# Performance work log

Measured on AMD Instinct MI355X. Metric: run time of the kernel, lower is better.

Reference implementation:

```python
import jax, jax.numpy as jnp
import numpy as np

N = 100000   # nodes (batched graph)
E = 1600000  # edges
G = 2048     # molecules in the batch
D_IN = 128
D_H = 128
MLP_H = 512


def setup_inputs() -> dict:
    key = jax.random.key(0)
    ks = jax.random.split(key, 20)

    def w(k, i, o):
        return (jax.random.normal(k, (i, o), jnp.float32) / np.sqrt(i)).astype(jnp.float32)

    feats = jax.random.normal(ks[0], (N, D_IN), jnp.float32)
    src = jax.random.randint(ks[1], (E,), 0, N)
    dst = jax.random.randint(ks[2], (E,), 0, N)
    graph_ids = jnp.sort(jax.random.randint(ks[3], (N,), 0, G))

    return {
        "feats": feats, "src": src, "dst": dst, "graph_ids": graph_ids,
        # 3 GraphConv layers
        "W0": w(ks[4], D_IN, D_H), "b0": jnp.zeros((D_H,), jnp.float32),
        "W1": w(ks[5], D_H, D_H),  "b1": jnp.zeros((D_H,), jnp.float32),
        "W2": w(ks[6], D_H, D_H),  "b2": jnp.zeros((D_H,), jnp.float32),
        # MLP head: D_H -> 512 -> 256 -> 1
        "Wm0": w(ks[7], D_H, MLP_H),       "bm0": jnp.zeros((MLP_H,), jnp.float32),
        "Wm1": w(ks[8], MLP_H, MLP_H // 2), "bm1": jnp.zeros((MLP_H // 2,), jnp.float32),
        "Wm2": w(ks[9], MLP_H // 2, 1),     "bm2": jnp.zeros((1,), jnp.float32),
    }


def reference(feats, src, dst, graph_ids, W0, b0, W1, b1, W2, b2,
              Wm0, bm0, Wm1, bm1, Wm2, bm2):
    ones_e = jnp.ones((E,), jnp.float32)
    # DGL GraphConv norm='both': D_out^{-1/2} on src, D_in^{-1/2} on dst; deg clamped to 1
    deg_out = jnp.maximum(jax.ops.segment_sum(ones_e, src, num_segments=N), 1.0)
    deg_in = jnp.maximum(jax.ops.segment_sum(ones_e, dst, num_segments=N), 1.0)
    inv_src = jax.lax.rsqrt(deg_out)[:, None]
    inv_dst = jax.lax.rsqrt(deg_in)[:, None]

    def gcn_layer(h, W, b):
        h = h * inv_src                                   # [N, D]
        m = jax.ops.segment_sum(h[src], dst, num_segments=N)  # gather-scatter over edges
        m = m * inv_dst
        return jax.nn.relu(jnp.dot(m, W) + b)

    h = gcn_layer(feats, W0, b0)
    h = gcn_layer(h, W1, b1)
    h = gcn_layer(h, W2, b2)

    # AvgPooling per graph
    counts = jnp.maximum(jax.ops.segment_sum(jnp.ones((N,), jnp.float32), graph_ids, num_segments=G), 1.0)
    emb = jax.ops.segment_sum(h, graph_ids, num_segments=G) / counts[:, None]  # [G, D_H]

    # MLP head (dropout = identity in eval)
    x = jax.nn.relu(jnp.dot(emb, Wm0) + bm0)
    x = jax.nn.relu(jnp.dot(x, Wm1) + bm1)
    return jnp.dot(x, Wm2) + bm2  # [G, 1]
```

## Files before the change

kernel.cpp:

```cpp
#include <hip/hip_runtime.h>


static inline int ceil_div(int a, int b){ return (a + b - 1) / b; }

#define B1 128
#define NBMAX 1024

__global__ __launch_bounds__(256) void bucket_count_kernel(
    const int* __restrict__ src, const int* __restrict__ dst,
    unsigned* __restrict__ cntA, unsigned* __restrict__ cntB,
    int E, int NB){
  __shared__ unsigned la[NBMAX], lb[NBMAX];
  int t = threadIdx.x;
  for (int i = t; i < NB; i += 256){ la[i] = 0u; lb[i] = 0u; }
  __syncthreads();
  int chunk = (E + B1 - 1) / B1;
  int e0 = blockIdx.x * chunk, e1 = min(e0 + chunk, E);
  for (int e = e0 + t; e < e1; e += 256){
    atomicAdd(&la[dst[e] >> 7], 1u);
    atomicAdd(&lb[src[e] >> 7], 1u);
  }
  __syncthreads();
  for (int i = t; i < NB; i += 256){
    cntA[(size_t)blockIdx.x * NB + i] = la[i];
    cntB[(size_t)blockIdx.x * NB + i] = lb[i];
  }
}

__global__ void scan_cols_kernel(unsigned* __restrict__ cntA, unsigned* __restrict__ cntB,
                                 unsigned* __restrict__ totals, int NB){
  int b = blockIdx.x * 256 + threadIdx.x;
  if (b >= NB) return;
  unsigned* cnt = blockIdx.y ? cntB : cntA;
  unsigned run = 0;
  for (int blk = 0; blk < B1; blk++){
    unsigned v = cnt[(size_t)blk * NB + b];
    cnt[(size_t)blk * NB + b] = run;
    run += v;
  }
  totals[(size_t)blockIdx.y * NB + b] = run;
}

__global__ void scan_base_kernel(const unsigned* __restrict__ totals,
                                 unsigned* __restrict__ baseA, unsigned* __restrict__ baseB,
                                 int NB, int E){
  __shared__ unsigned s[NBMAX];
  int t = threadIdx.x;
  for (int job = 0; job < 2; job++){
    unsigned* base = job ? baseB : baseA;
    unsigned x = (t < NB) ? totals[(size_t)job * NB + t] : 0u;
    s[t] = x;
    __syncthreads();
    for (int off = 1; off < NBMAX; off <<= 1){
      unsigned v = (t >= off) ? s[t - off] : 0u;
      __syncthreads();
      s[t] += v;
      __syncthreads();
    }
    if (t < NB) base[t] = s[t] - x;
    if (t == 0) base[NB] = (unsigned)E;
    __syncthreads();
  }
}

__global__ __launch_bounds__(256) void bucket_scatter_kernel(
    const int* __restrict__ src, const int* __restrict__ dst,
    const unsigned* __restrict__ cntA, const unsigned* __restrict__ cntB,
    const unsigned* __restrict__ baseA, const unsigned* __restrict__ baseB,
    int* __restrict__ bsrc_d, int* __restrict__ bdst_d, int* __restrict__ bsrc_s,
    int E, int NB){
  __shared__ unsigned curA[NBMAX], curB[NBMAX];
  int t = threadIdx.x;
  for (int i = t; i < NB; i += 256){
    curA[i] = baseA[i] + cntA[(size_t)blockIdx.x * NB + i];
    curB[i] = baseB[i] + cntB[(size_t)blockIdx.x * NB + i];
  }
  __syncthreads();
  int chunk = (E + B1 - 1) / B1;
  int e0 = blockIdx.x * chunk, e1 = min(e0 + chunk, E);
  for (int e = e0 + t; e < e1; e += 256){
    int s = src[e], d = dst[e];
    unsigned p = atomicAdd(&curA[d >> 7], 1u);
    bsrc_d[p] = s;
    bdst_d[p] = d;
    unsigned q = atomicAdd(&curB[s >> 7], 1u);
    bsrc_s[q] = s;
  }
}

__global__ __launch_bounds__(256) void csr_finalize_kernel(
    const int* __restrict__ bsrc_d, const int* __restrict__ bdst_d,
    const unsigned* __restrict__ baseA,
    int* __restrict__ row_ptr, float* __restrict__ inv_dst, int* __restrict__ col,
    int N, int E, int NB){
  __shared__ unsigned cnt[128];
  __shared__ unsigned scn[128];
  int b = blockIdx.x, t = threadIdx.x;
  int node0 = b << 7;
  int nn = min(128, N - node0);
  int e0 = (int)baseA[b], e1 = (int)baseA[b + 1];
  if (t < 128) cnt[t] = 0u;
  __syncthreads();
  for (int e = e0 + t; e < e1; e += 256)
    atomicAdd(&cnt[bdst_d[e] & 127], 1u);
  __syncthreads();
  unsigned mycnt = (t < 128) ? cnt[t] : 0u;
  if (t < 128) scn[t] = mycnt;
  __syncthreads();
  for (int off = 1; off < 128; off <<= 1){
    unsigned v = (t < 128 && t >= off) ? scn[t - off] : 0u;
    __syncthreads();
    if (t < 128) scn[t] += v;
    __syncthreads();
  }
  if (t < nn){
    unsigned excl = scn[t] - mycnt;
    row_ptr[node0 + t] = e0 + (int)excl;
    unsigned c = mycnt < 1u ? 1u : mycnt;
    inv_dst[node0 + t] = rsqrtf((float)c);
    cnt[t] = (unsigned)e0 + excl;
  }
  if (b == NB - 1 && t == 0) row_ptr[N] = E;
  __syncthreads();
  for (int e = e0 + t; e < e1; e += 256){
    unsigned p = atomicAdd(&cnt[bdst_d[e] & 127], 1u);
    col[p] = bsrc_d[e];
  }
}

__global__ __launch_bounds__(256) void degout_finalize_kernel(
    const int* __restrict__ bsrc_s, const unsigned* __restrict__ baseB,
    float* __restrict__ inv_src, int N){
  __shared__ unsigned cnt[128];
  int b = blockIdx.x, t = threadIdx.x;
  int node0 = b << 7;
  int nn = min(128, N - node0);
  int e0 = (int)baseB[b], e1 = (int)baseB[b + 1];
  if (t < 128) cnt[t] = 0u;
  __syncthreads();
  for (int e = e0 + t; e < e1; e += 256)
    atomicAdd(&cnt[bsrc_s[e] & 127], 1u);
  __syncthreads();
  if (t < nn){
    unsigned c = cnt[t] < 1u ? 1u : cnt[t];
    inv_src[node0 + t] = rsqrtf((float)c);
  }
}

__global__ void scale_rows_kernel(const float* __restrict__ in, const float* __restrict__ sc,
                                  float* __restrict__ out, int n4){
  int i = blockIdx.x*blockDim.x + threadIdx.x;
  if (i < n4){
    float4 v = ((const float4*)in)[i];
    float s = sc[i >> 5];
    v.x *= s; v.y *= s; v.z *= s; v.w *= s;
    ((float4*)out)[i] = v;
  }
}

__global__ __launch_bounds__(256) void csr_agg_kernel(
    const int* __restrict__ row_ptr, const int* __restrict__ col,
    const float* __restrict__ hs, float* __restrict__ agg, int N){
  int w = (int)((blockIdx.x*256u + threadIdx.x) >> 6);
  int lane = threadIdx.x & 63;
  if (w >= N) return;
  int r0 = __builtin_amdgcn_readfirstlane(row_ptr[w]);
  int r1 = __builtin_amdgcn_readfirstlane(row_ptr[w+1]);
  float ax0=0.f, ay0=0.f, ax1=0.f, ay1=0.f;
  float ax2=0.f, ay2=0.f, ax3=0.f, ay3=0.f;
  int e = r0;
  for (; e + 3 < r1; e += 4){
    int s0 = __builtin_amdgcn_readfirstlane(col[e]);
    int s1 = __builtin_amdgcn_readfirstlane(col[e+1]);
    int s2 = __builtin_amdgcn_readfirstlane(col[e+2]);
    int s3 = __builtin_amdgcn_readfirstlane(col[e+3]);
    float2 v0 = ((const float2*)(hs + (size_t)s0*128))[lane];
    float2 v1 = ((const float2*)(hs + (size_t)s1*128))[lane];
    float2 v2 = ((const float2*)(hs + (size_t)s2*128))[lane];
    float2 v3 = ((const float2*)(hs + (size_t)s3*128))[lane];
    ax0 += v0.x; ay0 += v0.y;
    ax1 += v1.x; ay1 += v1.y;
    ax2 += v2.x; ay2 += v2.y;
    ax3 += v3.x; ay3 += v3.y;
  }
  for (; e < r1; e++){
    int s0 = __builtin_amdgcn_readfirstlane(col[e]);
    float2 v0 = ((const float2*)(hs + (size_t)s0*128))[lane];
    ax0 += v0.x; ay0 += v0.y;
  }
  float2 r;
  r.x = (ax0 + ax1) + (ax2 + ax3);
  r.y = (ay0 + ay1) + (ay2 + ay3);
  ((float2*)(agg + (size_t)w*128))[lane] = r;
}

__global__ __launch_bounds__(256) void gemm_kernel(
    const float* __restrict__ A, const float* __restrict__ W,
    const float* __restrict__ bias, const float* __restrict__ row_scale,
    const float* __restrict__ out_scale, float* __restrict__ out,
    int M, int K, int Ncols, int do_relu){
  __shared__ float As[32][68];
  __shared__ float Bs[32][128];

  const int tid = threadIdx.x;
  const int tx = tid & 31;
  const int ty = tid >> 5;
  const int row0 = blockIdx.x * 64;
  const int col0 = blockIdx.y * 128;

  float acc[8][4];
  #pragma unroll
  for (int i = 0; i < 8; i++)
    #pragma unroll
    for (int j = 0; j < 4; j++) acc[i][j] = 0.f;

  for (int kb = 0; kb < K; kb += 32){
    #pragma unroll
    for (int i = 0; i < 2; i++){
      int flat = i*256 + tid;
      int m = flat >> 3, k4 = (flat & 7) << 2;
      int gm = row0 + m;
      float4 v = make_float4(0.f, 0.f, 0.f, 0.f);
      if (gm < M){
        v = *(const float4*)(A + (size_t)gm*K + kb + k4);
        if (row_scale){ float s = row_scale[gm]; v.x*=s; v.y*=s; v.z*=s; v.w*=s; }
      }
      As[k4+0][m] = v.x; As[k4+1][m] = v.y; As[k4+2][m] = v.z; As[k4+3][m] = v.w;
    }
    #pragma unroll
    for (int i = 0; i < 4; i++){
      int flat = i*256 + tid;
      int k = flat >> 5, j4 = (flat & 31) << 2;
      float4 v = *(const float4*)(W + (size_t)(kb + k)*Ncols + col0 + j4);
      *(float4*)&Bs[k][j4] = v;
    }
    __syncthreads();
    #pragma unroll
    for (int k = 0; k < 32; k++){
      float4 b = *(const float4*)&Bs[k][tx << 2];
      float a[8];
      #pragma unroll
      for (int i = 0; i < 8; i++) a[i] = As[k][ty*8 + i];
      #pragma unroll
      for (int i = 0; i < 8; i++){
        acc[i][0] = fmaf(a[i], b.x, acc[i][0]);
        acc[i][1] = fmaf(a[i], b.y, acc[i][1]);
        acc[i][2] = fmaf(a[i], b.z, acc[i][2]);
        acc[i][3] = fmaf(a[i], b.w, acc[i][3]);
      }
    }
    __syncthreads();
  }

  float4 bi = *(const float4*)(bias + col0 + (tx << 2));
  #pragma unroll
  for (int i = 0; i < 8; i++){
    int gm = row0 + ty*8 + i;
    if (gm < M){
      float4 v;
      v.x = acc[i][0] + bi.x; v.y = acc[i][1] + bi.y;
      v.z = acc[i][2] + bi.z; v.w = acc[i][3] + bi.w;
      if (do_relu){
        v.x = fmaxf(v.x, 0.f); v.y = fmaxf(v.y, 0.f);
        v.z = fmaxf(v.z, 0.f); v.w = fmaxf(v.w, 0.f);
      }
      if (out_scale){ float s = out_scale[gm]; v.x*=s; v.y*=s; v.z*=s; v.w*=s; }
      *(float4*)(out + (size_t)gm*Ncols + col0 + (tx << 2)) = v;
    }
  }
}

__global__ void pool_kernel(const float* __restrict__ h, const int* __restrict__ gid,
                            float* __restrict__ emb, int N, int G){
  int g = blockIdx.x;
  int lane = threadIdx.x;
  int lo = 0, hi = N;
  while (lo < hi){ int mid = (lo + hi) >> 1; if (gid[mid] < g) lo = mid + 1; else hi = mid; }
  int start = lo;
  hi = N;
  while (lo < hi){ int mid = (lo + hi) >> 1; if (gid[mid] <= g) lo = mid + 1; else hi = mid; }
  int end = lo;
  float ax = 0.f, ay = 0.f;
  for (int n = start; n < end; n++){
    float2 v = ((const float2*)(h + (size_t)n*128))[lane];
    ax += v.x; ay += v.y;
  }
  int c = end - start; if (c < 1) c = 1;
  float invc = 1.0f / (float)c;
  float2 r; r.x = ax * invc; r.y = ay * invc;
  ((float2*)(emb + (size_t)g*128))[lane] = r;
}

__global__ void final_dot_kernel(const float* __restrict__ x, const float* __restrict__ w,
                                 const float* __restrict__ b, float* __restrict__ out, int G){
  int idx = blockIdx.x*blockDim.x + threadIdx.x;
  int g = idx >> 6, lane = idx & 63;
  if (g >= G) return;
  float4 xv = ((const float4*)(x + (size_t)g*256))[lane];
  float4 wv = ((const float4*)w)[lane];
  float s = xv.x*wv.x + xv.y*wv.y + xv.z*wv.z + xv.w*wv.w;
  for (int off = 32; off > 0; off >>= 1) s += __shfl_down(s, off);
  if (lane == 0) out[g] = s + b[0];
}

extern "C" void kernel_launch(void* const* d_in, const int* in_sizes, int n_in,
                              void* d_out, int out_size, void* d_ws, size_t ws_size,
                              hipStream_t stream){
  const float* feats = (const float*)d_in[0];
  const int*   src   = (const int*)d_in[1];
  const int*   dst   = (const int*)d_in[2];
  const int*   gid   = (const int*)d_in[3];
  const float* W0 = (const float*)d_in[4];   const float* b0 = (const float*)d_in[5];
  const float* W1 = (const float*)d_in[6];   const float* b1 = (const float*)d_in[7];
  const float* W2 = (const float*)d_in[8];   const float* b2 = (const float*)d_in[9];
  const float* Wm0 = (const float*)d_in[10]; const float* bm0 = (const float*)d_in[11];
  const float* Wm1 = (const float*)d_in[12]; const float* bm1 = (const float*)d_in[13];
  const float* Wm2 = (const float*)d_in[14]; const float* bm2 = (const float*)d_in[15];
  float* out = (float*)d_out;

  const int E   = in_sizes[1];
  const int N   = in_sizes[3];
  const int G   = out_size;
  const int MH  = in_sizes[11];
  const int MH2 = in_sizes[13];
  const int NB  = ceil_div(N, 128);

  char* ws = (char*)d_ws;
  size_t off = 0;
  auto carve = [&](size_t bytes) -> char* {
    off = (off + 255) & ~(size_t)255;
    char* p = ws + off; off += bytes; return p;
  };
  float* inv_src = (float*)carve((size_t)N*4);
  float* inv_dst = (float*)carve((size_t)N*4);
  int* row_ptr = (int*)carve((size_t)(N+1)*4);
  int* col     = (int*)carve((size_t)E*4);
  float* hs  = (float*)carve((size_t)N*128*4);
  float* agg = (float*)carve((size_t)N*128*4);
  float* emb = (float*)carve((size_t)G*128*4);
  float* x1  = (float*)carve((size_t)G*MH*4);
  float* x2  = (float*)carve((size_t)G*MH2*4);

  unsigned* T = (unsigned*)agg;
  unsigned* cntA   = T;
  unsigned* cntB   = cntA + (size_t)B1*NB;
  unsigned* totals = cntB + (size_t)B1*NB;
  unsigned* baseA  = totals + 2*(size_t)NB;
  unsigned* baseB  = baseA + (NB+1);
  int* bsrc_d = (int*)(baseB + (NB+1));
  int* bdst_d = bsrc_d + E;
  int* bsrc_s = bdst_d + E;

  bucket_count_kernel<<<B1, 256, 0, stream>>>(src, dst, cntA, cntB, E, NB);
  scan_cols_kernel<<<dim3(ceil_div(NB,256), 2), 256, 0, stream>>>(cntA, cntB, totals, NB);
  scan_base_kernel<<<1, NBMAX, 0, stream>>>(totals, baseA, baseB, NB, E);
  bucket_scatter_kernel<<<B1, 256, 0, stream>>>(src, dst, cntA, cntB, baseA, baseB,
                                                bsrc_d, bdst_d, bsrc_s, E, NB);
  csr_finalize_kernel<<<NB, 256, 0, stream>>>(bsrc_d, bdst_d, baseA, row_ptr, inv_dst, col, N, E, NB);
  degout_finalize_kernel<<<NB, 256, 0, stream>>>(bsrc_s, baseB, inv_src, N);
  scale_rows_kernel<<<ceil_div(N*32,256), 256, 0, stream>>>(feats, inv_src, hs, N*32);

  const int agg_blocks = ceil_div(N*64, 256);
  dim3 ggrid(ceil_div(N,64), 1);
  csr_agg_kernel<<<agg_blocks, 256, 0, stream>>>(row_ptr, col, hs, agg, N);
  gemm_kernel<<<ggrid, 256, 0, stream>>>(agg, W0, b0, inv_dst, inv_src, hs, N, 128, 128, 1);
  csr_agg_kernel<<<agg_blocks, 256, 0, stream>>>(row_ptr, col, hs, agg, N);
  gemm_kernel<<<ggrid, 256, 0, stream>>>(agg, W1, b1, inv_dst, inv_src, hs, N, 128, 128, 1);
  csr_agg_kernel<<<agg_blocks, 256, 0, stream>>>(row_ptr, col, hs, agg, N);
  gemm_kernel<<<ggrid, 256, 0, stream>>>(agg, W2, b2, inv_dst, nullptr, hs, N, 128, 128, 1);
  pool_kernel<<<G, 64, 0, stream>>>(hs, gid, emb, N, G);
  gemm_kernel<<<dim3(ceil_div(G,64), MH/128),  256, 0, stream>>>(emb, Wm0, bm0, nullptr, nullptr, x1, G, 128, MH, 1);
  gemm_kernel<<<dim3(ceil_div(G,64), MH2/128), 256, 0, stream>>>(x1, Wm1, bm1, nullptr, nullptr, x2, G, MH, MH2, 1);
  final_dot_kernel<<<ceil_div(G*64,256), 256, 0, stream>>>(x2, Wm2, bm2, out, G);
}
```

Measured before the change: 825.8 us.

## Fuse CSR neighbor aggregation with dense layer GEMM into one kernel

Replaces the separate CSR aggregation and GEMM kernels per GCN layer with one kernel. Each block first aggregates 64 nodes' neighbor rows into shared memory (transposed, with inv_dst applied), then multiplies by the weight matrix with bias, ReLU and output scaling. The agg buffer is no longer written to and read back from global memory, and three launches are dropped. In exchange the kernel uses a larger shared-memory footprint (about 50KB), which may lower occupancy for the latency-bound gather phase. The GEMM phase now waits on the slowest of the block's 64 gather rows.

```diff
diff --git a/kernel.cpp b/kernel.cpp
--- a/kernel.cpp
+++ b/kernel.cpp
@@ -158,40 +158,103 @@
   }
 }
 
-__global__ __launch_bounds__(256) void csr_agg_kernel(
+__global__ __launch_bounds__(256) void agg_gemm_kernel(
     const int* __restrict__ row_ptr, const int* __restrict__ col,
-    const float* __restrict__ hs, float* __restrict__ agg, int N){
-  int w = (int)((blockIdx.x*256u + threadIdx.x) >> 6);
-  int lane = threadIdx.x & 63;
-  if (w >= N) return;
-  int r0 = __builtin_amdgcn_readfirstlane(row_ptr[w]);
-  int r1 = __builtin_amdgcn_readfirstlane(row_ptr[w+1]);
-  float ax0=0.f, ay0=0.f, ax1=0.f, ay1=0.f;
-  float ax2=0.f, ay2=0.f, ax3=0.f, ay3=0.f;
-  int e = r0;
-  for (; e + 3 < r1; e += 4){
-    int s0 = __builtin_amdgcn_readfirstlane(col[e]);
-    int s1 = __builtin_amdgcn_readfirstlane(col[e+1]);
-    int s2 = __builtin_amdgcn_readfirstlane(col[e+2]);
-    int s3 = __builtin_amdgcn_readfirstlane(col[e+3]);
-    float2 v0 = ((const float2*)(hs + (size_t)s0*128))[lane];
-    float2 v1 = ((const float2*)(hs + (size_t)s1*128))[lane];
-    float2 v2 = ((const float2*)(hs + (size_t)s2*128))[lane];
-    float2 v3 = ((const float2*)(hs + (size_t)s3*128))[lane];
-    ax0 += v0.x; ay0 += v0.y;
-    ax1 += v1.x; ay1 += v1.y;
-    ax2 += v2.x; ay2 += v2.y;
-    ax3 += v3.x; ay3 += v3.y;
-  }
-  for (; e < r1; e++){
-    int s0 = __builtin_amdgcn_readfirstlane(col[e]);
-    float2 v0 = ((const float2*)(hs + (size_t)s0*128))[lane];
-    ax0 += v0.x; ay0 += v0.y;
-  }
-  float2 r;
-  r.x = (ax0 + ax1) + (ax2 + ax3);
-  r.y = (ay0 + ay1) + (ay2 + ay3);
-  ((float2*)(agg + (size_t)w*128))[lane] = r;
+    const float* __restrict__ hs, const float* __restrict__ Wt,
+    const float* __restrict__ bias, const float* __restrict__ inv_dst,
+    const float* __restrict__ out_scale, float* __restrict__ out, int N){
+  __shared__ float As[128][68];
+  __shared__ float Bs[32][128];
+
+  const int tid = threadIdx.x;
+  const int wave = tid >> 6;
+  const int lane = tid & 63;
+  const int row0 = blockIdx.x * 64;
+
+  for (int mi = wave; mi < 64; mi += 4){
+    int node = row0 + mi;
+    float rx = 0.f, ry = 0.f;
+    if (node < N){
+      int r0 = __builtin_amdgcn_readfirstlane(row_ptr[node]);
+      int r1 = __builtin_amdgcn_readfirstlane(row_ptr[node+1]);
+      float ax0=0.f, ay0=0.f, ax1=0.f, ay1=0.f;
+      float ax2=0.f, ay2=0.f, ax3=0.f, ay3=0.f;
+      int e = r0;
+      for (; e + 3 < r1; e += 4){
+        int s0 = __builtin_amdgcn_readfirstlane(col[e]);
+        int s1 = __builtin_amdgcn_readfirstlane(col[e+1]);
+        int s2 = __builtin_amdgcn_readfirstlane(col[e+2]);
+        int s3 = __builtin_amdgcn_readfirstlane(col[e+3]);
+        float2 v0 = ((const float2*)(hs + (size_t)s0*128))[lane];
+        float2 v1 = ((const float2*)(hs + (size_t)s1*128))[lane];
+        float2 v2 = ((const float2*)(hs + (size_t)s2*128))[lane];
+        float2 v3 = ((const float2*)(hs + (size_t)s3*128))[lane];
+        ax0 += v0.x; ay0 += v0.y;
+        ax1 += v1.x; ay1 += v1.y;
+        ax2 += v2.x; ay2 += v2.y;
+        ax3 += v3.x; ay3 += v3.y;
+      }
+      for (; e < r1; e++){
+        int s0 = __builtin_amdgcn_readfirstlane(col[e]);
+        float2 v0 = ((const float2*)(hs + (size_t)s0*128))[lane];
+        ax0 += v0.x; ay0 += v0.y;
+      }
+      float idst = inv_dst[node];
+      rx = ((ax0 + ax1) + (ax2 + ax3)) * idst;
+      ry = ((ay0 + ay1) + (ay2 + ay3)) * idst;
+    }
+    As[2*lane][mi]   = rx;
+    As[2*lane+1][mi] = ry;
+  }
+  __syncthreads();
+
+  const int tx = tid & 31;
+  const int ty = tid >> 5;
+  float acc[8][4];
+  #pragma unroll
+  for (int i = 0; i < 8; i++)
+    #pragma unroll
+    for (int j = 0; j < 4; j++) acc[i][j] = 0.f;
+
+  for (int kb = 0; kb < 128; kb += 32){
+    #pragma unroll
+    for (int i = 0; i < 4; i++){
+      int flat = i*256 + tid;
+      int k = flat >> 5, j4 = (flat & 31) << 2;
+      *(float4*)&Bs[k][j4] = *(const float4*)(Wt + (size_t)(kb + k)*128 + j4);
+    }
+    __syncthreads();
+    #pragma unroll
+    for (int k = 0; k < 32; k++){
+      float4 b = *(const float4*)&Bs[k][tx << 2];
+      float a[8];
+      #pragma unroll
+      for (int i = 0; i < 8; i++) a[i] = As[kb + k][ty*8 + i];
+      #pragma unroll
+      for (int i = 0; i < 8; i++){
+        acc[i][0] = fmaf(a[i], b.x, acc[i][0]);
+        acc[i][1] = fmaf(a[i], b.y, acc[i][1]);
+        acc[i][2] = fmaf(a[i], b.z, acc[i][2]);
+        acc[i][3] = fmaf(a[i], b.w, acc[i][3]);
+      }
+    }
+    __syncthreads();
+  }
+
+  float4 bi = *(const float4*)(bias + (tx << 2));
+  #pragma unroll
+  for (int i = 0; i < 8; i++){
+    int gm = row0 + ty*8 + i;
+    if (gm < N){
+      float4 v;
+      v.x = fmaxf(acc[i][0] + bi.x, 0.f);
+      v.y = fmaxf(acc[i][1] + bi.y, 0.f);
+      v.z = fmaxf(acc[i][2] + bi.z, 0.f);
+      v.w = fmaxf(acc[i][3] + bi.w, 0.f);
+      if (out_scale){ float s = out_scale[gm]; v.x*=s; v.y*=s; v.z*=s; v.w*=s; }
+      *(float4*)(out + (size_t)gm*128 + (tx << 2)) = v;
+    }
+  }
 }
 
 __global__ __launch_bounds__(256) void gemm_kernel(
@@ -336,12 +399,12 @@
   int* row_ptr = (int*)carve((size_t)(N+1)*4);
   int* col     = (int*)carve((size_t)E*4);
   float* hs  = (float*)carve((size_t)N*128*4);
-  float* agg = (float*)carve((size_t)N*128*4);
+  float* h2  = (float*)carve((size_t)N*128*4);
   float* emb = (float*)carve((size_t)G*128*4);
   float* x1  = (float*)carve((size_t)G*MH*4);
   float* x2  = (float*)carve((size_t)G*MH2*4);
 
-  unsigned* T = (unsigned*)agg;
+  unsigned* T = (unsigned*)h2;
   unsigned* cntA   = T;
   unsigned* cntB   = cntA + (size_t)B1*NB;
   unsigned* totals = cntB + (size_t)B1*NB;
@@ -360,15 +423,11 @@
   degout_finalize_kernel<<<NB, 256, 0, stream>>>(bsrc_s, baseB, inv_src, N);
   scale_rows_kernel<<<ceil_div(N*32,256), 256, 0, stream>>>(feats, inv_src, hs, N*32);
 
-  const int agg_blocks = ceil_div(N*64, 256);
-  dim3 ggrid(ceil_div(N,64), 1);
-  csr_agg_kernel<<<agg_blocks, 256, 0, stream>>>(row_ptr, col, hs, agg, N);
-  gemm_kernel<<<ggrid, 256, 0, stream>>>(agg, W0, b0, inv_dst, inv_src, hs, N, 128, 128, 1);
-  csr_agg_kernel<<<agg_blocks, 256, 0, stream>>>(row_ptr, col, hs, agg, N);
-  gemm_kernel<<<ggrid, 256, 0, stream>>>(agg, W1, b1, inv_dst, inv_src, hs, N, 128, 128, 1);
-  csr_agg_kernel<<<agg_blocks, 256, 0, stream>>>(row_ptr, col, hs, agg, N);
-  gemm_kernel<<<ggrid, 256, 0, stream>>>(agg, W2, b2, inv_dst, nullptr, hs, N, 128, 128, 1);
-  pool_kernel<<<G, 64, 0, stream>>>(hs, gid, emb, N, G);
+  const int nblk = ceil_div(N, 64);
+  agg_gemm_kernel<<<nblk, 256, 0, stream>>>(row_ptr, col, hs, W0, b0, inv_dst, inv_src, h2, N);
+  agg_gemm_kernel<<<nblk, 256, 0, stream>>>(row_ptr, col, h2, W1, b1, inv_dst, inv_src, hs, N);
+  agg_gemm_kernel<<<nblk, 256, 0, stream>>>(row_ptr, col, hs, W2, b2, inv_dst, nullptr, h2, N);
+  pool_kernel<<<G, 64, 0, stream>>>(h2, gid, emb, N, G);
   gemm_kernel<<<dim3(ceil_div(G,64), MH/128),  256, 0, stream>>>(emb, Wm0, bm0, nullptr, nullptr, x1, G, 128, MH, 1);
   gemm_kernel<<<dim3(ceil_div(G,64), MH2/128), 256, 0, stream>>>(x1, Wm1, bm1, nullptr, nullptr, x2, G, MH, MH2, 1);
   final_dot_kernel<<<ceil_div(G*64,256), 256, 0, stream>>>(x2, Wm2, bm2, out, G);
```

Result: slower. 1.023 ms (+23.9%).
